# Performance work log

Hardware: AMD Instinct MI355X
Metric: run time of the kernel (lower is better)

Reference implementation:

```python
import jax, jax.numpy as jnp
import numpy as np

OUT_FEATURES = 4096
IN_FEATURES = 4096


def _unpack_int4_symmetric(packed, n_values):
    # packed: uint8-valued int32 array; each byte holds two 4-bit values:
    # high nibble first, low nibble second (packing was (v0 << 4) | v1 with v in [0,15]=q+8)
    high = (packed >> 4) & 15
    low = packed & 15
    interleaved = jnp.stack([high, low], axis=-1).reshape(-1)[:n_values]
    # symmetric: quantized value q = nibble - 8, zero_point = 0
    return interleaved.astype(jnp.float32) - 8.0


def setup_inputs() -> dict:
    key = jax.random.key(0)
    k1, k2, k3, k4, k5 = jax.random.split(key, 5)
    x = jax.random.normal(k1, (4, 2048, IN_FEATURES), dtype=jnp.float32)
    packed_w = jax.random.randint(k2, (OUT_FEATURES * IN_FEATURES // 2,), 0, 256, dtype=jnp.int32)
    packed_b = jax.random.randint(k3, (OUT_FEATURES // 2,), 0, 256, dtype=jnp.int32)
    scale_w = jax.random.uniform(k4, (), dtype=jnp.float32) * 0.01 + 1e-4
    scale_b = jax.random.uniform(k5, (), dtype=jnp.float32) * 0.01 + 1e-4
    return {"x": x, "packed_w": packed_w, "packed_b": packed_b,
            "scale_w": scale_w, "scale_b": scale_b}


def reference(x, packed_w, packed_b, scale_w, scale_b):
    # dequantize weight: scale * (q - zero_point), zero_point = 0 (symmetric)
    qw = _unpack_int4_symmetric(packed_w, OUT_FEATURES * IN_FEATURES)
    W = (scale_w * qw).reshape(OUT_FEATURES, IN_FEATURES)  # [O, I]
    qb = _unpack_int4_symmetric(packed_b, OUT_FEATURES)
    b = scale_b * qb  # [O]
    # F.linear(x, W, b) = x @ W.T + b
    return jnp.einsum('bsi,oi->bso', x, W) + b
```

## Files before the change

### kernel.cpp

```cpp
#include <hip/hip_runtime.h>
#include <hip/hip_bf16.h>

#define M_DIM 8192
#define N_DIM 4096
#define K_DIM 4096

typedef _Float16 f16;
typedef _Float16 f16x8 __attribute__((ext_vector_type(8)));
typedef float f32x4 __attribute__((ext_vector_type(4)));

__device__ __forceinline__ void lds_async16(void* lds, const void* g) {
    __builtin_amdgcn_global_load_lds(
        (const __attribute__((address_space(1))) void*)(void*)g,
        (__attribute__((address_space(3))) void*)lds, 16, 0, 0);
}

__global__ __launch_bounds__(256) void cvt_x_kernel(const float* __restrict__ x, f16* __restrict__ xh) {
    size_t idx  = (size_t)blockIdx.x * 256 + threadIdx.x;
    size_t base = idx * 8;
    const float4* xp = (const float4*)(x + base);
    float4 v0 = xp[0], v1 = xp[1];
    f16x8 h;
    h[0] = (f16)v0.x; h[1] = (f16)v0.y; h[2] = (f16)v0.z; h[3] = (f16)v0.w;
    h[4] = (f16)v1.x; h[5] = (f16)v1.y; h[6] = (f16)v1.z; h[7] = (f16)v1.w;
    *(f16x8*)(xh + base) = h;
}

__global__ __launch_bounds__(256) void cvt_w_kernel(const int* __restrict__ pw, f16* __restrict__ wh) {
    size_t idx = (size_t)blockIdx.x * 256 + threadIdx.x;
    int4 v = ((const int4*)pw)[idx];
    f16x8 h;
    int a;
    a = v.x; h[0] = (f16)(((a >> 4) & 15) - 8); h[1] = (f16)((a & 15) - 8);
    a = v.y; h[2] = (f16)(((a >> 4) & 15) - 8); h[3] = (f16)((a & 15) - 8);
    a = v.z; h[4] = (f16)(((a >> 4) & 15) - 8); h[5] = (f16)((a & 15) - 8);
    a = v.w; h[6] = (f16)(((a >> 4) & 15) - 8); h[7] = (f16)((a & 15) - 8);
    *(f16x8*)(wh + idx * 8) = h;
}

__global__ __launch_bounds__(256) void gemm_f16(const f16* __restrict__ A, const f16* __restrict__ B,
                                                const int* __restrict__ pb,
                                                const float* __restrict__ psw, const float* __restrict__ psb,
                                                float* __restrict__ out) {
    __shared__ f16 As[128 * 32];
    __shared__ f16 Bs[128 * 32];

    const int tid  = threadIdx.x;
    const int wave = tid >> 6;
    const int lane = tid & 63;
    const int wm   = wave >> 1;
    const int wn   = wave & 1;
    const int quad = lane >> 4;
    const int l16  = lane & 15;

    const int mbase = blockIdx.y * 128;
    const int nbase = blockIdx.x * 128;

    const int srow = lane >> 2;
    const int scol = ((lane & 3) ^ ((lane >> 3) & 3)) * 8;

    const f16* aP0 = A + (size_t)(mbase + wave * 32 + srow) * K_DIM + scol;
    const f16* aP1 = aP0 + (size_t)16 * K_DIM;
    const f16* bP0 = B + (size_t)(nbase + wave * 32 + srow) * K_DIM + scol;
    const f16* bP1 = bP0 + (size_t)16 * K_DIM;

    f16* aD0 = As + (wave * 2 + 0) * 512;
    f16* aD1 = As + (wave * 2 + 1) * 512;
    f16* bD0 = Bs + (wave * 2 + 0) * 512;
    f16* bD1 = Bs + (wave * 2 + 1) * 512;

    f32x4 acc[4][4] = {};

    const int aslot = (l16 * 4 + (quad ^ ((l16 >> 1) & 3))) * 8;

    for (int k0 = 0; k0 < K_DIM; k0 += 32) {
        lds_async16(aD0, aP0);
        lds_async16(aD1, aP1);
        lds_async16(bD0, bP0);
        lds_async16(bD1, bP1);
        aP0 += 32; aP1 += 32; bP0 += 32; bP1 += 32;
        __syncthreads();

        f16x8 af[4], bf[4];
#pragma unroll
        for (int mt = 0; mt < 4; mt++)
            af[mt] = *(const f16x8*)&As[(wm * 4 + mt) * 512 + aslot];
#pragma unroll
        for (int nt = 0; nt < 4; nt++)
            bf[nt] = *(const f16x8*)&Bs[(wn * 4 + nt) * 512 + aslot];

#pragma unroll
        for (int mt = 0; mt < 4; mt++)
#pragma unroll
            for (int nt = 0; nt < 4; nt++)
                acc[mt][nt] = __builtin_amdgcn_mfma_f32_16x16x32_f16(af[mt], bf[nt], acc[mt][nt], 0, 0, 0);

        __syncthreads();
    }

    const float sw = *psw;
    const float sb = *psb;

#pragma unroll
    for (int nt = 0; nt < 4; nt++) {
        const int gcol = nbase + wn * 64 + nt * 16 + l16;
        const int p    = pb[gcol >> 1];
        const int nib  = (gcol & 1) ? (p & 15) : ((p >> 4) & 15);
        const float bias = sb * (float)(nib - 8);
#pragma unroll
        for (int mt = 0; mt < 4; mt++) {
            const int grow = mbase + wm * 64 + mt * 16 + quad * 4;
            float* o = out + (size_t)grow * N_DIM + gcol;
#pragma unroll
            for (int r = 0; r < 4; r++)
                o[(size_t)r * N_DIM] = sw * acc[mt][nt][r] + bias;
        }
    }
}

__global__ __launch_bounds__(256) void gemm_fallback(const float* __restrict__ x, const int* __restrict__ pw,
                                                     const int* __restrict__ pb,
                                                     const float* __restrict__ psw, const float* __restrict__ psb,
                                                     float* __restrict__ out) {
    __shared__ float As[16][17];
    __shared__ float Bs[16][17];
    const int tx = threadIdx.x & 15, ty = threadIdx.x >> 4;
    const int row = blockIdx.y * 16 + ty;
    const int col = blockIdx.x * 16 + tx;
    float acc = 0.f;
    for (int k0 = 0; k0 < K_DIM; k0 += 16) {
        As[ty][tx] = x[(size_t)row * K_DIM + k0 + tx];
        const int nrow = blockIdx.x * 16 + ty;
        const int k = k0 + tx;
        const int p = pw[((size_t)nrow * K_DIM + k) >> 1];
        const int nib = (k & 1) ? (p & 15) : ((p >> 4) & 15);
        Bs[ty][tx] = (float)(nib - 8);
        __syncthreads();
#pragma unroll
        for (int kk = 0; kk < 16; kk++)
            acc += As[ty][kk] * Bs[tx][kk];
        __syncthreads();
    }
    const float sw = *psw, sb = *psb;
    const int p = pb[col >> 1];
    const int nib = (col & 1) ? (p & 15) : ((p >> 4) & 15);
    out[(size_t)row * N_DIM + col] = sw * acc + sb * (float)(nib - 8);
}

extern "C" void kernel_launch(void* const* d_in, const int* in_sizes, int n_in,
                              void* d_out, int out_size, void* d_ws, size_t ws_size,
                              hipStream_t stream) {
    (void)in_sizes; (void)n_in; (void)out_size;
    const float* x   = (const float*)d_in[0];
    const int*   pw  = (const int*)d_in[1];
    const int*   pb  = (const int*)d_in[2];
    const float* psw = (const float*)d_in[3];
    const float* psb = (const float*)d_in[4];
    float* out = (float*)d_out;

    const size_t xh_bytes = (size_t)M_DIM * K_DIM * sizeof(f16);
    const size_t wh_bytes = (size_t)N_DIM * K_DIM * sizeof(f16);

    if (ws_size >= xh_bytes + wh_bytes) {
        f16* xh = (f16*)d_ws;
        f16* wh = (f16*)((char*)d_ws + xh_bytes);
        cvt_x_kernel<<<(M_DIM * (size_t)K_DIM) / 8 / 256, 256, 0, stream>>>(x, xh);
        cvt_w_kernel<<<((size_t)N_DIM * K_DIM / 2) / 4 / 256, 256, 0, stream>>>(pw, wh);
        gemm_f16<<<dim3(N_DIM / 128, M_DIM / 128), 256, 0, stream>>>(xh, wh, pb, psw, psb, out);
    } else {
        gemm_fallback<<<dim3(N_DIM / 16, M_DIM / 16), 256, 0, stream>>>(x, pw, pb, psw, psb, out);
    }
}
```

Measured before the change: 547.7 us.

## Switch GEMM to 32x32x16 MFMA with K-tile 64 and XOR-swizzled LDS

Replaces the 16x16x32 MFMA tiling with 32x32x16 MFMA instructions, so each wave computes its 64x64 sub-tile with 2x2 larger accumulators. The K tile per iteration doubles from 32 to 64, halving the number of barrier pairs and loop iterations. The LDS layout uses a new 8-way XOR swizzle matched to the new fragment reads. Larger MFMAs give more FLOPs per LDS byte read, at the cost of double the LDS footprint, which may lower occupancy.

Result: faster. 506.7 us (-7.5%).

```diff
diff --git a/kernel.cpp b/kernel.cpp
--- a/kernel.cpp
+++ b/kernel.cpp
@@ -7,7 +7,7 @@
 
 typedef _Float16 f16;
 typedef _Float16 f16x8 __attribute__((ext_vector_type(8)));
-typedef float f32x4 __attribute__((ext_vector_type(4)));
+typedef float f32x16 __attribute__((ext_vector_type(16)));
 
 __device__ __forceinline__ void lds_async16(void* lds, const void* g) {
     __builtin_amdgcn_global_load_lds(
@@ -42,58 +42,70 @@
                                                 const int* __restrict__ pb,
                                                 const float* __restrict__ psw, const float* __restrict__ psb,
                                                 float* __restrict__ out) {
-    __shared__ f16 As[128 * 32];
-    __shared__ f16 Bs[128 * 32];
+    __shared__ f16 As[128 * 64];
+    __shared__ f16 Bs[128 * 64];
 
     const int tid  = threadIdx.x;
     const int wave = tid >> 6;
     const int lane = tid & 63;
     const int wm   = wave >> 1;
     const int wn   = wave & 1;
-    const int quad = lane >> 4;
-    const int l16  = lane & 15;
+    const int half = lane >> 5;
+    const int l32  = lane & 31;
 
     const int mbase = blockIdx.y * 128;
     const int nbase = blockIdx.x * 128;
 
-    const int srow = lane >> 2;
-    const int scol = ((lane & 3) ^ ((lane >> 3) & 3)) * 8;
+    const int srow = lane >> 3;
+    const int scol = ((lane & 7) ^ srow) * 8;
 
-    const f16* aP0 = A + (size_t)(mbase + wave * 32 + srow) * K_DIM + scol;
-    const f16* aP1 = aP0 + (size_t)16 * K_DIM;
-    const f16* bP0 = B + (size_t)(nbase + wave * 32 + srow) * K_DIM + scol;
-    const f16* bP1 = bP0 + (size_t)16 * K_DIM;
+    const f16* aP[4]; const f16* bP[4];
+    f16* aD[4]; f16* bD[4];
+#pragma unroll
+    for (int j = 0; j < 4; j++) {
+        aP[j] = A + (size_t)(mbase + wave * 32 + j * 8 + srow) * K_DIM + scol;
+        bP[j] = B + (size_t)(nbase + wave * 32 + j * 8 + srow) * K_DIM + scol;
+        aD[j] = As + (wave * 4 + j) * 512;
+        bD[j] = Bs + (wave * 4 + j) * 512;
+    }
 
-    f16* aD0 = As + (wave * 2 + 0) * 512;
-    f16* aD1 = As + (wave * 2 + 1) * 512;
-    f16* bD0 = Bs + (wave * 2 + 0) * 512;
-    f16* bD1 = Bs + (wave * 2 + 1) * 512;
+    f32x16 acc[2][2] = {};
 
-    f32x4 acc[4][4] = {};
+    int abase[2], bbase[2], arr[2], brr[2];
+#pragma unroll
+    for (int t = 0; t < 2; t++) {
+        int ra = wm * 64 + t * 32 + l32;
+        int rb = wn * 64 + t * 32 + l32;
+        abase[t] = (ra >> 3) * 512 + (ra & 7) * 64;
+        arr[t]   = ra & 7;
+        bbase[t] = (rb >> 3) * 512 + (rb & 7) * 64;
+        brr[t]   = rb & 7;
+    }
 
-    const int aslot = (l16 * 4 + (quad ^ ((l16 >> 1) & 3))) * 8;
-
-    for (int k0 = 0; k0 < K_DIM; k0 += 32) {
-        lds_async16(aD0, aP0);
-        lds_async16(aD1, aP1);
-        lds_async16(bD0, bP0);
-        lds_async16(bD1, bP1);
-        aP0 += 32; aP1 += 32; bP0 += 32; bP1 += 32;
+    for (int k0 = 0; k0 < K_DIM; k0 += 64) {
+#pragma unroll
+        for (int j = 0; j < 4; j++) {
+            lds_async16(aD[j], aP[j]);
+            lds_async16(bD[j], bP[j]);
+            aP[j] += 64; bP[j] += 64;
+        }
         __syncthreads();
 
-        f16x8 af[4], bf[4];
 #pragma unroll
-        for (int mt = 0; mt < 4; mt++)
-            af[mt] = *(const f16x8*)&As[(wm * 4 + mt) * 512 + aslot];
+        for (int kk = 0; kk < 64; kk += 16) {
+            const int kc = (kk >> 3) + half;
+            f16x8 af[2], bf[2];
 #pragma unroll
-        for (int nt = 0; nt < 4; nt++)
-            bf[nt] = *(const f16x8*)&Bs[(wn * 4 + nt) * 512 + aslot];
-
+            for (int t = 0; t < 2; t++) {
+                af[t] = *(const f16x8*)&As[abase[t] + (kc ^ arr[t]) * 8];
+                bf[t] = *(const f16x8*)&Bs[bbase[t] + (kc ^ brr[t]) * 8];
+            }
 #pragma unroll
-        for (int mt = 0; mt < 4; mt++)
+            for (int mt = 0; mt < 2; mt++)
 #pragma unroll
-            for (int nt = 0; nt < 4; nt++)
-                acc[mt][nt] = __builtin_amdgcn_mfma_f32_16x16x32_f16(af[mt], bf[nt], acc[mt][nt], 0, 0, 0);
+                for (int nt = 0; nt < 2; nt++)
+                    acc[mt][nt] = __builtin_amdgcn_mfma_f32_32x32x16_f16(af[mt], bf[nt], acc[mt][nt], 0, 0, 0);
+        }
 
         __syncthreads();
     }
@@ -102,18 +114,21 @@
     const float sb = *psb;
 
 #pragma unroll
-    for (int nt = 0; nt < 4; nt++) {
-        const int gcol = nbase + wn * 64 + nt * 16 + l16;
+    for (int nt = 0; nt < 2; nt++) {
+        const int gcol = nbase + wn * 64 + nt * 32 + l32;
         const int p    = pb[gcol >> 1];
         const int nib  = (gcol & 1) ? (p & 15) : ((p >> 4) & 15);
         const float bias = sb * (float)(nib - 8);
 #pragma unroll
-        for (int mt = 0; mt < 4; mt++) {
-            const int grow = mbase + wm * 64 + mt * 16 + quad * 4;
-            float* o = out + (size_t)grow * N_DIM + gcol;
+        for (int mt = 0; mt < 2; mt++) {
+            const int rbase = mbase + wm * 64 + mt * 32 + half * 4;
 #pragma unroll
-            for (int r = 0; r < 4; r++)
-                o[(size_t)r * N_DIM] = sw * acc[mt][nt][r] + bias;
+            for (int g = 0; g < 4; g++) {
+                float* o = out + (size_t)(rbase + g * 8) * N_DIM + gcol;
+#pragma unroll
+                for (int r = 0; r < 4; r++)
+                    o[(size_t)r * N_DIM] = sw * acc[mt][nt][g * 4 + r] + bias;
+            }
         }
     }
 }
```
